# Performance work log

Measured on AMD Instinct MI355X. Metric: run time of the kernel, lower is better.

## Reference

```python
import jax, jax.numpy as jnp
import numpy as np

NUM_HEADS = 16

def setup_inputs() -> dict:
    key = jax.random.key(0)
    k1, k2, k3 = jax.random.split(key, 3)
    B, S, D = 2, 2048, 1024
    x = jax.random.normal(k1, (B, S, D), dtype=jnp.float32)
    Wqkv = jax.random.normal(k2, (D, 3 * D), dtype=jnp.float32) * (1.0 / np.sqrt(D))
    bqkv = jnp.zeros((3 * D,), dtype=jnp.float32)
    Wo = jax.random.normal(k3, (D, D), dtype=jnp.float32) * (1.0 / np.sqrt(D))
    bo = jnp.zeros((D,), dtype=jnp.float32)
    return {"x": x, "Wqkv": Wqkv, "bqkv": bqkv, "Wo": Wo, "bo": bo}

def reference(x, Wqkv, bqkv, Wo, bo):
    B, S, D = x.shape
    H = NUM_HEADS
    hd = D // H
    # qkv projection, split into per-head q, k, v: [B, H, S, hd]
    qkv = (x @ Wqkv + bqkv).reshape(B, S, H, 3 * hd).transpose(0, 2, 1, 3)
    q, k, v = jnp.split(qkv, 3, axis=-1)
    # causal attention scores [B, H, S, S]
    scores = jnp.einsum('bhqd,bhkd->bhqk', q, k)
    causal = jnp.tril(jnp.ones((S, S), dtype=bool))  # True = keep
    scores = jnp.where(causal, scores, -jnp.inf)
    attn = jax.nn.softmax(scores / np.sqrt(hd).astype(np.float32), axis=-1)
    # dropout is identity in eval mode
    ctx = jnp.einsum('bhqk,bhkd->bhqd', attn, v)  # [B, H, S, hd]
    ctx = ctx.transpose(0, 2, 1, 3).reshape(B, S, D)
    return ctx @ Wo + bo
```

## Files before the change

### kernel.cpp

```cpp
#include <hip/hip_runtime.h>


typedef __attribute__((ext_vector_type(8))) __bf16 bf16x8;
typedef __attribute__((ext_vector_type(4))) float f32x4;
typedef __attribute__((ext_vector_type(4))) short short4v;

__device__ __forceinline__ unsigned short f2bf(float f) {
    union { float f; unsigned u; } v; v.f = f;
    unsigned r = v.u + 0x7fffu + ((v.u >> 16) & 1u);
    return (unsigned short)(r >> 16);
}

__device__ __forceinline__ unsigned pack_bf16x2_trunc(float a, float b) {
#if defined(__HIP_DEVICE_COMPILE__)
    return __builtin_amdgcn_perm(__builtin_bit_cast(unsigned, a),
                                 __builtin_bit_cast(unsigned, b), 0x03020706u);
#else
    return 0u;
#endif
}

__device__ __forceinline__ float fast_exp2(float x) {
#if defined(__HIP_DEVICE_COMPILE__)
    return __builtin_amdgcn_exp2f(x);
#else
    return x;
#endif
}

__device__ __forceinline__ void async_copy16(const unsigned short* g, unsigned short* l) {
    __builtin_amdgcn_global_load_lds(
        (const __attribute__((address_space(1))) unsigned int*)g,
        (__attribute__((address_space(3))) unsigned int*)l, 16, 0, 0);
}

__device__ __forceinline__ f32x4 mfma16x16x16(short4v a, short4v b, f32x4 c) {
#if defined(__HIP_DEVICE_COMPILE__)
    return __builtin_amdgcn_mfma_f32_16x16x16bf16_1k(a, b, c, 0, 0, 0);
#else
    return c;
#endif
}

__global__ __launch_bounds__(256) void convert_f32_bf16(
    const float* __restrict__ in, unsigned short* __restrict__ out)
{
    size_t i = ((size_t)blockIdx.x * 256 + threadIdx.x) * 8;
    float4 v0 = *(const float4*)(in + i);
    float4 v1 = *(const float4*)(in + i + 4);
    ushort4 a, b;
    a.x = f2bf(v0.x); a.y = f2bf(v0.y); a.z = f2bf(v0.z); a.w = f2bf(v0.w);
    b.x = f2bf(v1.x); b.y = f2bf(v1.y); b.z = f2bf(v1.z); b.w = f2bf(v1.w);
    *(ushort4*)(out + i) = a;
    *(ushort4*)(out + i + 4) = b;
}

__global__ __launch_bounds__(256) void transpose_f32_bf16(
    const float* __restrict__ in, unsigned short* __restrict__ out, int K, int N)
{
    __shared__ float T[64][65];
    const int tid = threadIdx.x;
    const int n0 = blockIdx.x * 64, k0 = blockIdx.y * 64;
#pragma unroll
    for (int i = 0; i < 4; i++) {
        int idx = tid + i * 256;
        int r = idx >> 4, c4 = (idx & 15) * 4;
        float4 v = *(const float4*)(in + (size_t)(k0 + r) * N + n0 + c4);
        T[r][c4 + 0] = v.x; T[r][c4 + 1] = v.y; T[r][c4 + 2] = v.z; T[r][c4 + 3] = v.w;
    }
    __syncthreads();
#pragma unroll
    for (int i = 0; i < 4; i++) {
        int idx = tid + i * 256;
        int n = idx >> 4, k4 = (idx & 15) * 4;
        ushort4 o;
        o.x = f2bf(T[k4 + 0][n]); o.y = f2bf(T[k4 + 1][n]);
        o.z = f2bf(T[k4 + 2][n]); o.w = f2bf(T[k4 + 3][n]);
        *(ushort4*)(out + (size_t)(n0 + n) * K + k0 + k4) = o;
    }
}

__global__ __launch_bounds__(256) void transpose_v(
    const unsigned short* __restrict__ vrow, unsigned short* __restrict__ vt)
{
    __shared__ unsigned short T[64 * 72];
    const int tid = threadIdx.x;
    const int bh = blockIdx.y;
    const int s0 = blockIdx.x * 64;
    const unsigned short* src = vrow + ((size_t)bh * 2048 + s0) * 64;
    unsigned short* dst = vt + (size_t)bh * 64 * 2048 + s0;
#pragma unroll
    for (int i = 0; i < 2; i++) {
        int idx = tid + i * 256;
        int s = idx >> 3, dg = (idx & 7) * 8;
        *(uint4*)&T[s * 72 + dg] = *(const uint4*)(src + s * 64 + dg);
    }
    __syncthreads();
#pragma unroll
    for (int i = 0; i < 2; i++) {
        int idx = tid + i * 256;
        int d = idx >> 3, sg = (idx & 7) * 8;
        ushort4 a, b;
        a.x = T[(sg + 0) * 72 + d]; a.y = T[(sg + 1) * 72 + d];
        a.z = T[(sg + 2) * 72 + d]; a.w = T[(sg + 3) * 72 + d];
        b.x = T[(sg + 4) * 72 + d]; b.y = T[(sg + 5) * 72 + d];
        b.z = T[(sg + 6) * 72 + d]; b.w = T[(sg + 7) * 72 + d];
        *(ushort4*)(dst + (size_t)d * 2048 + sg) = a;
        *(ushort4*)(dst + (size_t)d * 2048 + sg + 4) = b;
    }
}

__global__ __launch_bounds__(256) void gemm_qkv_bf(
    const unsigned short* __restrict__ Xbf,
    const unsigned short* __restrict__ WT,
    const float* __restrict__ bias,
    unsigned short* __restrict__ qws, unsigned short* __restrict__ kws,
    unsigned short* __restrict__ vrow)
{
    const int K = 1024;
    __shared__ __align__(16) unsigned short smem[128 * 136];
    unsigned short* As = smem;
    unsigned short* Bs = smem + 8192;
    const int tid = threadIdx.x;
    const int m0 = blockIdx.y * 128, n0 = blockIdx.x * 128;
    const int wave = tid >> 6, lane = tid & 63;
    const int wm = (wave >> 1) * 64, wn = (wave & 1) * 64;
    const int quad = lane >> 4, l16 = lane & 15;
    const int lrow = lane >> 3, lgrp = lane & 7;
    const int sg = lgrp ^ lrow;

    f32x4 acc[4][4];
    const f32x4 Z4 = {0.f, 0.f, 0.f, 0.f};
#pragma unroll
    for (int i = 0; i < 4; i++)
#pragma unroll
        for (int j = 0; j < 4; j++) acc[i][j] = Z4;

    for (int k0 = 0; k0 < K; k0 += 64) {
        __syncthreads();
#pragma unroll
        for (int c = 0; c < 4; c++) {
            int nb = (wave * 4 + c) * 8;
            async_copy16(Xbf + (size_t)(m0 + nb + lrow) * K + k0 + sg * 8, &As[nb * 64]);
            async_copy16(WT  + (size_t)(n0 + nb + lrow) * K + k0 + sg * 8, &Bs[nb * 64]);
        }
        __syncthreads();
#pragma unroll
        for (int kk = 0; kk < 2; kk++) {
            int pg = ((kk * 4 + quad) ^ (l16 & 7)) * 8;
            bf16x8 af[4], bfr[4];
#pragma unroll
            for (int mi = 0; mi < 4; mi++) af[mi] = *(const bf16x8*)&As[(wm + mi * 16 + l16) * 64 + pg];
#pragma unroll
            for (int ni = 0; ni < 4; ni++) bfr[ni] = *(const bf16x8*)&Bs[(wn + ni * 16 + l16) * 64 + pg];
#pragma unroll
            for (int mi = 0; mi < 4; mi++)
#pragma unroll
                for (int ni = 0; ni < 4; ni++)
                    acc[mi][ni] = __builtin_amdgcn_mfma_f32_16x16x32_bf16(af[mi], bfr[ni], acc[mi][ni], 0, 0, 0);
        }
    }
    __syncthreads();
#pragma unroll
    for (int ni = 0; ni < 4; ni++) {
        int colL = wn + ni * 16 + l16;
        int col = n0 + colL;
        int t = (col % 192) >> 6;
        float bv = bias[col];
        float scl = (t == 1) ? 0.18033688f : 1.0f;
#pragma unroll
        for (int mi = 0; mi < 4; mi++)
#pragma unroll
            for (int r = 0; r < 4; r++) {
                int row = wm + mi * 16 + quad * 4 + r;
                smem[row * 136 + colL] = f2bf((acc[mi][ni][r] + bv) * scl);
            }
    }
    __syncthreads();
#pragma unroll
    for (int i = 0; i < 8; i++) {
        int idx = tid + i * 256;
        int row = idx >> 4, g = idx & 15;
        int colL = g * 8;
        uint4 w = *(const uint4*)&smem[row * 136 + colL];
        int col = n0 + colL;
        int h = col / 192, rem = col % 192, t = rem >> 6, d = rem & 63;
        int grow = m0 + row;
        int b = grow >> 11, s = grow & 2047;
        unsigned short* dst = (t == 0) ? qws : (t == 1) ? kws : vrow;
        *(uint4*)(dst + ((size_t)(b * 16 + h) * 2048 + s) * 64 + d) = w;
    }
}

__global__ __launch_bounds__(256) void attn(
    const unsigned short* __restrict__ qws, const unsigned short* __restrict__ kws,
    const unsigned short* __restrict__ vtws, unsigned short* __restrict__ ctx)
{
    __shared__ __align__(16) unsigned short Qs[128 * 64];
    __shared__ __align__(16) unsigned short Ks[64 * 64];
    __shared__ __align__(16) unsigned short Vt[64][72];

    const int tid = threadIdx.x;
    const int wave = tid >> 6, lane = tid & 63, quad = lane >> 4, l16 = lane & 15;
    const int lrow = lane >> 3, lgrp = lane & 7;
    const int sg = lgrp ^ lrow;

    const int i = blockIdx.x;
    const int idx = i & 255;
    const int tile = (i < 256) ? (15 - (idx >> 5)) : (idx >> 5);
    const int bh = idx & 31;
    const int q0 = tile * 128;

    const unsigned short* Q  = qws + (size_t)bh * 2048 * 64;
    const unsigned short* Kp = kws + (size_t)bh * 2048 * 64;
    const unsigned short* Vp = vtws + (size_t)bh * 64 * 2048;

#pragma unroll
    for (int c = 0; c < 4; c++) {
        int rb = (wave * 4 + c) * 8;
        async_copy16(Q + (size_t)(q0 + rb + lrow) * 64 + sg * 8, &Qs[rb * 64]);
    }

    const int wq = wave * 32;
    f32x4 o[4][2];
    const f32x4 Z4 = {0.f, 0.f, 0.f, 0.f};
#pragma unroll
    for (int dt = 0; dt < 4; dt++)
#pragma unroll
        for (int qt = 0; qt < 2; qt++) o[dt][qt] = Z4;
    float lsum[2] = {0.f, 0.f};

    const int jmax = tile * 2 + 2;
    for (int j = 0; j < jmax; j++) {
        const int kb0 = j * 64;
        __syncthreads();
#pragma unroll
        for (int c = 0; c < 2; c++) {
            int rb = (wave * 2 + c) * 8;
            async_copy16(Kp + (size_t)(kb0 + rb + lrow) * 64 + sg * 8, &Ks[rb * 64]);
        }
#pragma unroll
        for (int ii = 0; ii < 2; ii++) {
            int id2 = tid + ii * 256;
            int row = id2 >> 3, c = (id2 & 7) * 8;
            *(uint4*)&Vt[row][c] = *(const uint4*)(Vp + (size_t)row * 2048 + kb0 + c);
        }
        __syncthreads();

        if (kb0 <= q0 + wq + 31) {
            f32x4 sc[4][2];
#pragma unroll
            for (int kt = 0; kt < 4; kt++)
#pragma unroll
                for (int qt = 0; qt < 2; qt++) sc[kt][qt] = Z4;
#pragma unroll
            for (int kk = 0; kk < 2; kk++) {
                int pg = ((kk * 4 + quad) ^ (l16 & 7)) * 8;
                bf16x8 ak[4], bq[2];
#pragma unroll
                for (int kt = 0; kt < 4; kt++) ak[kt] = *(const bf16x8*)&Ks[(kt * 16 + l16) * 64 + pg];
#pragma unroll
                for (int qt = 0; qt < 2; qt++) bq[qt] = *(const bf16x8*)&Qs[(wq + qt * 16 + l16) * 64 + pg];
#pragma unroll
                for (int kt = 0; kt < 4; kt++)
#pragma unroll
                    for (int qt = 0; qt < 2; qt++)
                        sc[kt][qt] = __builtin_amdgcn_mfma_f32_16x16x32_bf16(ak[kt], bq[qt], sc[kt][qt], 0, 0, 0);
            }
            short4v pb[4][2];
            if (kb0 + 63 <= q0 + wq) {
#pragma unroll
                for (int qt = 0; qt < 2; qt++)
#pragma unroll
                    for (int kt = 0; kt < 4; kt++) {
                        float p0 = fast_exp2(sc[kt][qt][0]);
                        float p1 = fast_exp2(sc[kt][qt][1]);
                        float p2 = fast_exp2(sc[kt][qt][2]);
                        float p3 = fast_exp2(sc[kt][qt][3]);
                        lsum[qt] += (p0 + p1) + (p2 + p3);
                        uint2 uu;
                        uu.x = pack_bf16x2_trunc(p0, p1);
                        uu.y = pack_bf16x2_trunc(p2, p3);
                        pb[kt][qt] = __builtin_bit_cast(short4v, uu);
                    }
            } else {
#pragma unroll
                for (int qt = 0; qt < 2; qt++) {
                    int qg = q0 + wq + qt * 16 + l16;
#pragma unroll
                    for (int kt = 0; kt < 4; kt++) {
                        float p[4];
#pragma unroll
                        for (int r = 0; r < 4; r++) {
                            int key = kb0 + kt * 16 + quad * 4 + r;
                            float t = fast_exp2(sc[kt][qt][r]);
                            p[r] = (key <= qg) ? t : 0.f;
                        }
                        lsum[qt] += (p[0] + p[1]) + (p[2] + p[3]);
                        uint2 uu;
                        uu.x = pack_bf16x2_trunc(p[0], p[1]);
                        uu.y = pack_bf16x2_trunc(p[2], p[3]);
                        pb[kt][qt] = __builtin_bit_cast(short4v, uu);
                    }
                }
            }
#pragma unroll
            for (int kt = 0; kt < 4; kt++) {
#pragma unroll
                for (int dt = 0; dt < 4; dt++) {
                    short4v av = *(const short4v*)&Vt[dt * 16 + l16][kt * 16 + quad * 4];
#pragma unroll
                    for (int qt = 0; qt < 2; qt++)
                        o[dt][qt] = mfma16x16x16(av, pb[kt][qt], o[dt][qt]);
                }
            }
        }
    }
#pragma unroll
    for (int qt = 0; qt < 2; qt++) {
        lsum[qt] += __shfl_xor(lsum[qt], 16);
        lsum[qt] += __shfl_xor(lsum[qt], 32);
    }
    const int b = bh >> 4, h = bh & 15;
#pragma unroll
    for (int qt = 0; qt < 2; qt++) {
        int qg = q0 + wq + qt * 16 + l16;
        float inv = 1.0f / lsum[qt];
#pragma unroll
        for (int dt = 0; dt < 4; dt++) {
            ushort4 ov;
            ov.x = f2bf(o[dt][qt][0] * inv);
            ov.y = f2bf(o[dt][qt][1] * inv);
            ov.z = f2bf(o[dt][qt][2] * inv);
            ov.w = f2bf(o[dt][qt][3] * inv);
            *(ushort4*)(ctx + (size_t)(b * 2048 + qg) * 1024 + h * 64 + dt * 16 + quad * 4) = ov;
        }
    }
}

__global__ __launch_bounds__(256) void gemm_out(
    const unsigned short* __restrict__ Ctx, const unsigned short* __restrict__ WT,
    const float* __restrict__ bias, float* __restrict__ Out)
{
    const int K = 1024, N = 1024;
    __shared__ __align__(16) unsigned short As[128 * 64];
    __shared__ __align__(16) unsigned short Bs[128 * 64];
    const int tid = threadIdx.x;
    const int m0 = blockIdx.y * 128, n0 = blockIdx.x * 128;
    const int wave = tid >> 6, lane = tid & 63;
    const int wm = (wave >> 1) * 64, wn = (wave & 1) * 64;
    const int quad = lane >> 4, l16 = lane & 15;
    const int lrow = lane >> 3, lgrp = lane & 7;
    const int sg = lgrp ^ lrow;

    f32x4 acc[4][4];
    const f32x4 Z4 = {0.f, 0.f, 0.f, 0.f};
#pragma unroll
    for (int i = 0; i < 4; i++)
#pragma unroll
        for (int j = 0; j < 4; j++) acc[i][j] = Z4;

    for (int k0 = 0; k0 < K; k0 += 64) {
        __syncthreads();
#pragma unroll
        for (int c = 0; c < 4; c++) {
            int nb = (wave * 4 + c) * 8;
            async_copy16(Ctx + (size_t)(m0 + nb + lrow) * K + k0 + sg * 8, &As[nb * 64]);
            async_copy16(WT  + (size_t)(n0 + nb + lrow) * K + k0 + sg * 8, &Bs[nb * 64]);
        }
        __syncthreads();
#pragma unroll
        for (int kk = 0; kk < 2; kk++) {
            int pg = ((kk * 4 + quad) ^ (l16 & 7)) * 8;
            bf16x8 af[4], bfr[4];
#pragma unroll
            for (int mi = 0; mi < 4; mi++) af[mi] = *(const bf16x8*)&As[(wm + mi * 16 + l16) * 64 + pg];
#pragma unroll
            for (int ni = 0; ni < 4; ni++) bfr[ni] = *(const bf16x8*)&Bs[(wn + ni * 16 + l16) * 64 + pg];
#pragma unroll
            for (int mi = 0; mi < 4; mi++)
#pragma unroll
                for (int ni = 0; ni < 4; ni++)
                    acc[mi][ni] = __builtin_amdgcn_mfma_f32_16x16x32_bf16(af[mi], bfr[ni], acc[mi][ni], 0, 0, 0);
        }
    }
#pragma unroll
    for (int mi = 0; mi < 4; mi++)
#pragma unroll
        for (int ni = 0; ni < 4; ni++) {
            int col = n0 + wn + ni * 16 + l16;
            float bv = bias[col];
#pragma unroll
            for (int r = 0; r < 4; r++) {
                int row = m0 + wm + mi * 16 + quad * 4 + r;
                Out[(size_t)row * N + col] = acc[mi][ni][r] + bv;
            }
        }
}

extern "C" void kernel_launch(void* const* d_in, const int* in_sizes, int n_in,
                              void* d_out, int out_size, void* d_ws, size_t ws_size,
                              hipStream_t stream) {
    const float* x    = (const float*)d_in[0];
    const float* Wqkv = (const float*)d_in[1];
    const float* bqkv = (const float*)d_in[2];
    const float* Wo   = (const float*)d_in[3];
    const float* bo   = (const float*)d_in[4];
    float* out = (float*)d_out;

    const size_t R = 4194304;
    unsigned short* q    = (unsigned short*)d_ws;
    unsigned short* k    = q + R;
    unsigned short* vrow = k + R;
    unsigned short* ctx  = vrow + R;
    unsigned short* xbf  = ctx + R;
    unsigned short* vt   = xbf;
    unsigned short* wqkvT = ctx;
    unsigned short* woT   = q;

    convert_f32_bf16<<<dim3(2048), 256, 0, stream>>>(x, xbf);
    transpose_f32_bf16<<<dim3(48, 16), 256, 0, stream>>>(Wqkv, wqkvT, 1024, 3072);
    gemm_qkv_bf<<<dim3(24, 32), 256, 0, stream>>>(xbf, wqkvT, bqkv, q, k, vrow);
    transpose_v<<<dim3(32, 32), 256, 0, stream>>>(vrow, vt);
    attn<<<dim3(512), 256, 0, stream>>>(q, k, vt, ctx);
    transpose_f32_bf16<<<dim3(16, 16), 256, 0, stream>>>(Wo, woT, 1024, 1024);
    gemm_out<<<dim3(8, 32), 256, 0, stream>>>(ctx, woT, bo, out);
}
```

Before: 205.9 us.

## Double-buffer K/V tiles in attention and halve gemm_out M tile

The attention kernel now keeps two LDS buffers for the K and V^T tiles. While the current 64-key block is being computed, it issues the async K copy and register-staged V loads for the next block, and stores V into the other buffer after the math. This drops one barrier per iteration and hides global load latency behind the MFMA work, at the cost of extra LDS and registers. Separately, gemm_out uses a 64-row M tile instead of 128, doubling the grid to 512 blocks to fill more CUs, with less reuse of each loaded B tile.

```diff
diff --git a/kernel.cpp b/kernel.cpp
--- a/kernel.cpp
+++ b/kernel.cpp
@@ -197,8 +197,8 @@
     const unsigned short* __restrict__ vtws, unsigned short* __restrict__ ctx)
 {
     __shared__ __align__(16) unsigned short Qs[128 * 64];
-    __shared__ __align__(16) unsigned short Ks[64 * 64];
-    __shared__ __align__(16) unsigned short Vt[64][72];
+    __shared__ __align__(16) unsigned short Ks[2][64 * 64];
+    __shared__ __align__(16) unsigned short Vt[2][64][72];
 
     const int tid = threadIdx.x;
     const int wave = tid >> 6, lane = tid & 63, quad = lane >> 4, l16 = lane & 15;
@@ -220,6 +220,17 @@
         int rb = (wave * 4 + c) * 8;
         async_copy16(Q + (size_t)(q0 + rb + lrow) * 64 + sg * 8, &Qs[rb * 64]);
     }
+#pragma unroll
+    for (int c = 0; c < 2; c++) {
+        int rb = (wave * 2 + c) * 8;
+        async_copy16(Kp + (size_t)(rb + lrow) * 64 + sg * 8, &Ks[0][rb * 64]);
+    }
+#pragma unroll
+    for (int ii = 0; ii < 2; ii++) {
+        int id2 = tid + ii * 256;
+        int row = id2 >> 3, c = (id2 & 7) * 8;
+        *(uint4*)&Vt[0][row][c] = *(const uint4*)(Vp + (size_t)row * 2048 + c);
+    }
 
     const int wq = wave * 32;
     f32x4 o[4][2];
@@ -232,20 +243,25 @@
 
     const int jmax = tile * 2 + 2;
     for (int j = 0; j < jmax; j++) {
+        const int cur = j & 1, nxt = cur ^ 1;
+        __syncthreads();
         const int kb0 = j * 64;
-        __syncthreads();
-#pragma unroll
-        for (int c = 0; c < 2; c++) {
-            int rb = (wave * 2 + c) * 8;
-            async_copy16(Kp + (size_t)(kb0 + rb + lrow) * 64 + sg * 8, &Ks[rb * 64]);
-        }
-#pragma unroll
-        for (int ii = 0; ii < 2; ii++) {
-            int id2 = tid + ii * 256;
-            int row = id2 >> 3, c = (id2 & 7) * 8;
-            *(uint4*)&Vt[row][c] = *(const uint4*)(Vp + (size_t)row * 2048 + kb0 + c);
-        }
-        __syncthreads();
+        const bool pf = (j + 1) < jmax;
+        uint4 vreg[2];
+        if (pf) {
+            const int kb1 = kb0 + 64;
+#pragma unroll
+            for (int ii = 0; ii < 2; ii++) {
+                int id2 = tid + ii * 256;
+                int row = id2 >> 3, c = (id2 & 7) * 8;
+                vreg[ii] = *(const uint4*)(Vp + (size_t)row * 2048 + kb1 + c);
+            }
+#pragma unroll
+            for (int c = 0; c < 2; c++) {
+                int rb = (wave * 2 + c) * 8;
+                async_copy16(Kp + (size_t)(kb1 + rb + lrow) * 64 + sg * 8, &Ks[nxt][rb * 64]);
+            }
+        }
 
         if (kb0 <= q0 + wq + 31) {
             f32x4 sc[4][2];
@@ -258,7 +274,7 @@
                 int pg = ((kk * 4 + quad) ^ (l16 & 7)) * 8;
                 bf16x8 ak[4], bq[2];
 #pragma unroll
-                for (int kt = 0; kt < 4; kt++) ak[kt] = *(const bf16x8*)&Ks[(kt * 16 + l16) * 64 + pg];
+                for (int kt = 0; kt < 4; kt++) ak[kt] = *(const bf16x8*)&Ks[cur][(kt * 16 + l16) * 64 + pg];
 #pragma unroll
                 for (int qt = 0; qt < 2; qt++) bq[qt] = *(const bf16x8*)&Qs[(wq + qt * 16 + l16) * 64 + pg];
 #pragma unroll
@@ -308,11 +324,20 @@
             for (int kt = 0; kt < 4; kt++) {
 #pragma unroll
                 for (int dt = 0; dt < 4; dt++) {
-                    short4v av = *(const short4v*)&Vt[dt * 16 + l16][kt * 16 + quad * 4];
+                    short4v av = *(const short4v*)&Vt[cur][dt * 16 + l16][kt * 16 + quad * 4];
 #pragma unroll
                     for (int qt = 0; qt < 2; qt++)
                         o[dt][qt] = mfma16x16x16(av, pb[kt][qt], o[dt][qt]);
                 }
+            }
+        }
+
+        if (pf) {
+#pragma unroll
+            for (int ii = 0; ii < 2; ii++) {
+                int id2 = tid + ii * 256;
+                int row = id2 >> 3, c = (id2 & 7) * 8;
+                *(uint4*)&Vt[nxt][row][c] = vreg[ii];
             }
         }
     }
@@ -343,49 +368,53 @@
     const float* __restrict__ bias, float* __restrict__ Out)
 {
     const int K = 1024, N = 1024;
-    __shared__ __align__(16) unsigned short As[128 * 64];
+    __shared__ __align__(16) unsigned short As[64 * 64];
     __shared__ __align__(16) unsigned short Bs[128 * 64];
     const int tid = threadIdx.x;
-    const int m0 = blockIdx.y * 128, n0 = blockIdx.x * 128;
+    const int m0 = blockIdx.y * 64, n0 = blockIdx.x * 128;
     const int wave = tid >> 6, lane = tid & 63;
-    const int wm = (wave >> 1) * 64, wn = (wave & 1) * 64;
+    const int wm = (wave >> 1) * 32, wn = (wave & 1) * 64;
     const int quad = lane >> 4, l16 = lane & 15;
     const int lrow = lane >> 3, lgrp = lane & 7;
     const int sg = lgrp ^ lrow;
 
-    f32x4 acc[4][4];
+    f32x4 acc[2][4];
     const f32x4 Z4 = {0.f, 0.f, 0.f, 0.f};
 #pragma unroll
-    for (int i = 0; i < 4; i++)
+    for (int i = 0; i < 2; i++)
 #pragma unroll
         for (int j = 0; j < 4; j++) acc[i][j] = Z4;
 
     for (int k0 = 0; k0 < K; k0 += 64) {
         __syncthreads();
 #pragma unroll
+        for (int c = 0; c < 2; c++) {
+            int nb = (wave * 2 + c) * 8;
+            async_copy16(Ctx + (size_t)(m0 + nb + lrow) * K + k0 + sg * 8, &As[nb * 64]);
+        }
+#pragma unroll
         for (int c = 0; c < 4; c++) {
             int nb = (wave * 4 + c) * 8;
-            async_copy16(Ctx + (size_t)(m0 + nb + lrow) * K + k0 + sg * 8, &As[nb * 64]);
-            async_copy16(WT  + (size_t)(n0 + nb + lrow) * K + k0 + sg * 8, &Bs[nb * 64]);
+            async_copy16(WT + (size_t)(n0 + nb + lrow) * K + k0 + sg * 8, &Bs[nb * 64]);
         }
         __syncthreads();
 #pragma unroll
         for (int kk = 0; kk < 2; kk++) {
             int pg = ((kk * 4 + quad) ^ (l16 & 7)) * 8;
-            bf16x8 af[4], bfr[4];
-#pragma unroll
-            for (int mi = 0; mi < 4; mi++) af[mi] = *(const bf16x8*)&As[(wm + mi * 16 + l16) * 64 + pg];
+            bf16x8 af[2], bfr[4];
+#pragma unroll
+            for (int mi = 0; mi < 2; mi++) af[mi] = *(const bf16x8*)&As[(wm + mi * 16 + l16) * 64 + pg];
 #pragma unroll
             for (int ni = 0; ni < 4; ni++) bfr[ni] = *(const bf16x8*)&Bs[(wn + ni * 16 + l16) * 64 + pg];
 #pragma unroll
-            for (int mi = 0; mi < 4; mi++)
+            for (int mi = 0; mi < 2; mi++)
 #pragma unroll
                 for (int ni = 0; ni < 4; ni++)
                     acc[mi][ni] = __builtin_amdgcn_mfma_f32_16x16x32_bf16(af[mi], bfr[ni], acc[mi][ni], 0, 0, 0);
         }
     }
 #pragma unroll
-    for (int mi = 0; mi < 4; mi++)
+    for (int mi = 0; mi < 2; mi++)
 #pragma unroll
         for (int ni = 0; ni < 4; ni++) {
             int col = n0 + wn + ni * 16 + l16;
@@ -424,5 +453,5 @@
     transpose_v<<<dim3(32, 32), 256, 0, stream>>>(vrow, vt);
     attn<<<dim3(512), 256, 0, stream>>>(q, k, vt, ctx);
     transpose_f32_bf16<<<dim3(16, 16), 256, 0, stream>>>(Wo, woT, 1024, 1024);
-    gemm_out<<<dim3(8, 32), 256, 0, stream>>>(ctx, woT, bo, out);
-}
+    gemm_out<<<dim3(8, 64), 256, 0, stream>>>(ctx, woT, bo, out);
+}
```

Result: no change. 203.9 us (-1.0%).
